# Optimization experiments

Measured on AMD Instinct MI355X. Metric: run time of the kernel, lower is better.

The kernel has to match this reference:

```python
import jax, jax.numpy as jnp
import numpy as np

NEG_CLAMP = -100.0  # torch F.binary_cross_entropy clamps log terms at -100


def _ccl_labels(fg):
    """4-connectivity connected-component labeling of a [H,W] bool mask.
    Labels are assigned in raster-scan first-encounter order, matching
    scipy.ndimage.label with the default structure. Background = 0.
    Implemented as min-index label propagation to a fixed point: each
    component ends up tagged with the min flat index of its pixels (its
    first raster-scan pixel), then roots are ranked by cumsum to get 1..num.
    """
    H, W = fg.shape
    INF = H * W  # sentinel larger than any flat index
    idx = jnp.arange(INF, dtype=jnp.int32).reshape(H, W)
    init = jnp.where(fg, idx, INF)

    def step(x):
        up = jnp.concatenate([x[1:], jnp.full((1, W), INF, x.dtype)], axis=0)
        down = jnp.concatenate([jnp.full((1, W), INF, x.dtype), x[:-1]], axis=0)
        left = jnp.concatenate([x[:, 1:], jnp.full((H, 1), INF, x.dtype)], axis=1)
        right = jnp.concatenate([jnp.full((H, 1), INF, x.dtype), x[:, :-1]], axis=1)
        m = jnp.minimum(jnp.minimum(up, down), jnp.minimum(left, right))
        return jnp.where(fg, jnp.minimum(x, m), INF)

    def cond(carry):
        return carry[1]

    def body(carry):
        x, _ = carry
        nx = step(x)
        return nx, jnp.any(nx != x)

    x, _ = jax.lax.while_loop(cond, body, (init, jnp.array(True)))

    flat = x.reshape(-1)
    fgf = fg.reshape(-1)
    # a pixel is the root of its component iff its propagated tag == its own index
    is_root = fgf & (flat == jnp.arange(INF, dtype=jnp.int32))
    rank = jnp.cumsum(is_root.astype(jnp.int32))  # rank[r] = scipy label of root r
    labels = jnp.where(fgf, rank[jnp.clip(flat, 0, INF - 1)], 0)
    return labels.reshape(H, W)


def _target_map(fg):
    """Replicates: labels == labels.flatten()[1:].argmax() + 1 (faithful to source,
    including its quirky use of argmax position as the selected label value)."""
    labels = _ccl_labels(fg)
    lf = labels.reshape(-1)
    v = jnp.argmax(lf[1:]) + 1  # first occurrence of max, like numpy argmax
    return (labels == v).astype(jnp.float32)


def setup_inputs() -> dict:
    key = jax.random.key(0)
    pred = jax.random.uniform(key, (32, 1, 512, 512), dtype=jnp.float32)
    return {"pred": pred}


def reference(pred):
    fg = pred[:, 0] >= 0.5  # [N,H,W] bool
    target = jax.vmap(_target_map)(fg)[:, None]  # [N,1,H,W] float
    logp = jnp.maximum(jnp.log(pred), NEG_CLAMP)
    log1mp = jnp.maximum(jnp.log1p(-pred), NEG_CLAMP)
    return -jnp.mean(target * logp + (1.0 - target) * log1mp)
```

## Files before the change

kernel.cpp:

```cpp
#include <hip/hip_runtime.h>
#include <math.h>

#define IMG_W 512
#define IMG_H 512
#define HW (IMG_W * IMG_H)
#define LOGHW 18
#define NIMG 32
#define NTOT (NIMG * HW)
#define TILE 64
#define TPI 64
#define NTILE (NIMG * TPI)
#define CPI 64
#define NSCHUNK (NIMG * CPI)
#define VBORD ((8 - 1) * IMG_H)
#define BORD_PER_IMG (VBORD + (8 - 1) * IMG_W)
#define NBORD (NIMG * BORD_PER_IMG)


__device__ __forceinline__ void uf_unite(int* L, int a, int b) {
    while (true) {
        int p = ((volatile int*)L)[a];
        while (p != a) { a = p; p = ((volatile int*)L)[a]; }
        p = ((volatile int*)L)[b];
        while (p != b) { b = p; p = ((volatile int*)L)[b]; }
        if (a == b) return;
        if (a < b) { int t = a; a = b; b = t; }
        int old = atomicMin(&L[a], b);
        if (old == a) return;
        a = old;
    }
}

__global__ __launch_bounds__(512) void k_local(const float* __restrict__ pred,
                                               int* __restrict__ L,
                                               float* __restrict__ partials) {
    __shared__ int lab[TILE * TILE];
    __shared__ float sred[512];
    int tile = blockIdx.x;
    int img = tile >> 6;
    int t = tile & (TPI - 1);
    int ty = t >> 3, tx = t & 7;
    int baseLocal = (ty * TILE) * IMG_W + tx * TILE;
    const float* pi = pred + ((size_t)img << LOGHW);
    int* Li = L + ((size_t)img << LOGHW);
    int tid = threadIdx.x;
    int lane = tid & 63, wave = tid >> 6;

    float acc = 0.0f;
#pragma unroll
    for (int j = 0; j < 8; j++) {
        int row = wave + j * 8;
        float p = pi[baseLocal + row * IMG_W + lane];
        acc += fmaxf(__logf(1.0f - p), -100.0f);
        bool fg = (p >= 0.5f);
        unsigned long long bal = __ballot(fg);
        unsigned long long starts = bal & ~(bal << 1);
        unsigned long long maskle =
            (lane == 63) ? ~0ULL : ((1ULL << (lane + 1)) - 1ULL);
        int lb = -1;
        if (fg) {
            unsigned long long pre = starts & maskle;
            lb = row * TILE + (63 - __builtin_clzll(pre));
        }
        lab[row * TILE + lane] = lb;
    }
    __syncthreads();
#pragma unroll
    for (int j = 0; j < 8; j++) {
        int row = wave + j * 8;
        if (row == 0) continue;
        int i = row * TILE + lane;
        bool c = (lab[i] >= 0) && (lab[i - TILE] >= 0);
        unsigned long long cb = __ballot(c);
        unsigned long long cs = cb & ~(cb << 1);
        if ((cs >> lane) & 1ULL) uf_unite(lab, i, i - TILE);
    }
    __syncthreads();
#pragma unroll
    for (int j = 0; j < 2; j++) {
        int i4 = (tid + j * 512) * 4;
        int ly = i4 >> 6, lx = i4 & 63;
        int4 o;
        int* op = (int*)&o;
#pragma unroll
        for (int k = 0; k < 4; k++) {
            int x = i4 + k;
            int p = lab[x];
            if (p < 0) op[k] = -1;
            else {
                while (p != x) {
                    int g = lab[p];
                    lab[x] = g;
                    x = g;
                    p = lab[x];
                }
                op[k] = baseLocal + (x >> 6) * IMG_W + (x & 63);
            }
        }
        *(int4*)(Li + baseLocal + ly * IMG_W + lx) = o;
    }
    sred[tid] = acc;
    __syncthreads();
    for (int s = 256; s > 0; s >>= 1) {
        if (tid < s) sred[tid] += sred[tid + s];
        __syncthreads();
    }
    if (tid == 0) partials[blockIdx.x] = sred[0];
}

__global__ void k_border(int* __restrict__ L) {
    int gid = blockIdx.x * blockDim.x + threadIdx.x;
    int img = gid / BORD_PER_IMG;
    int r = gid - img * BORD_PER_IMG;
    int* Li = L + ((size_t)img << LOGHW);
    int a, b;
    if (r < VBORD) {
        int k = r >> 9, y = r & 511;
        int x = k * TILE + (TILE - 1);
        a = y * IMG_W + x; b = a + 1;
    } else {
        int r2 = r - VBORD;
        int k = r2 >> 9, x = r2 & 511;
        int y = k * TILE + (TILE - 1);
        a = y * IMG_W + x; b = a + IMG_W;
    }
    bool c = (Li[a] >= 0) && (Li[b] >= 0);
    unsigned long long cb = __ballot(c);
    unsigned long long cs = cb & ~(cb << 1);
    if ((cs >> (threadIdx.x & 63)) & 1ULL) uf_unite(Li, a, b);
}

__global__ __launch_bounds__(256) void k_stats(const int* __restrict__ L,
                                               int* __restrict__ cntArr,
                                               int* __restrict__ maxArr,
                                               int* __restrict__ minArr) {
    __shared__ int s1[256], s2[256], s3[256];
    int chunk = blockIdx.x;
    int img = chunk >> 6;
    int baseL = (chunk & 63) * 4096;
    const int* Li = L + ((size_t)img << LOGHW);
    int t = threadIdx.x;
    int cnt = 0, mx = -1, mn = HW;
#pragma unroll
    for (int j = 0; j < 4; j++) {
        int off = baseL + (t + j * 256) * 4;
        int4 l4 = *(const int4*)(Li + off);
        const int* lp = (const int*)&l4;
#pragma unroll
        for (int k = 0; k < 4; k++) {
            int local = off + k;
            int p = lp[k];
            bool root = (p == local);
            cnt += root ? 1 : 0;
            if (root && local > mx) mx = local;
            if (p >= 0 && local >= 1 && local < mn) mn = local;
        }
    }
    s1[t] = cnt; s2[t] = mx; s3[t] = mn;
    __syncthreads();
    for (int s = 128; s > 0; s >>= 1) {
        if (t < s) {
            s1[t] += s1[t + s];
            s2[t] = max(s2[t], s2[t + s]);
            s3[t] = min(s3[t], s3[t + s]);
        }
        __syncthreads();
    }
    if (t == 0) { cntArr[chunk] = s1[0]; maxArr[chunk] = s2[0]; minArr[chunk] = s3[0]; }
}

__global__ __launch_bounds__(256) void k_rv(const int* __restrict__ cntArr,
                                            const int* __restrict__ maxArr,
                                            const int* __restrict__ minArr,
                                            const int* __restrict__ L,
                                            int* __restrict__ rv) {
    __shared__ int sc[256], sm[256], sn[256];
    __shared__ int sel_chunk, sel_base, result;
    int img = blockIdx.x, t = threadIdx.x;
    int cnt = (t < CPI) ? cntArr[img * CPI + t] : 0;
    sc[t] = cnt;
    sm[t] = (t < CPI) ? maxArr[img * CPI + t] : -1;
    sn[t] = (t < CPI) ? minArr[img * CPI + t] : HW;
    if (t == 0) result = -2;
    __syncthreads();
    for (int off = 1; off < 256; off <<= 1) {
        int v2 = (t >= off) ? sc[t - off] : 0;
        __syncthreads();
        sc[t] += v2;
        __syncthreads();
    }
    int num = sc[255];
    int inc = sc[t], exc = inc - cnt;
    for (int s = 128; s > 0; s >>= 1) {
        if (t < s) { sm[t] = max(sm[t], sm[t + s]); sn[t] = min(sn[t], sn[t + s]); }
        __syncthreads();
    }
    int last_root = sm[0], minFg = sn[0];
    int v;
    if (last_root >= 1) v = last_root;
    else if (last_root == 0) v = (minFg < HW) ? minFg : 1;
    else v = 1;
    if (v >= 1 && v <= num) {
        if (exc < v && v <= inc) { sel_chunk = t; sel_base = exc; }
        __syncthreads();
        int c = sel_chunk, base = sel_base;
        const int* Li = L + ((size_t)img << LOGHW);
        int baseL = c * 4096;
        int f[16];
        int sum = 0;
#pragma unroll
        for (int j = 0; j < 4; j++) {
            int off = baseL + t * 16 + j * 4;
            int4 l4 = *(const int4*)(Li + off);
            const int* lp = (const int*)&l4;
#pragma unroll
            for (int k = 0; k < 4; k++) {
                f[j * 4 + k] = (lp[k] == off + k) ? 1 : 0;
                sum += f[j * 4 + k];
            }
        }
        __syncthreads();
        sc[t] = sum;
        __syncthreads();
        for (int off = 1; off < 256; off <<= 1) {
            int v2 = (t >= off) ? sc[t - off] : 0;
            __syncthreads();
            sc[t] += v2;
            __syncthreads();
        }
        int exc2 = sc[t] - sum;
        int need = v - base;
        if (exc2 < need && need <= sc[t]) {
            int run = exc2;
#pragma unroll
            for (int k = 0; k < 16; k++) {
                run += f[k];
                if (run == need) { result = baseL + t * 16 + k; break; }
            }
        }
        __syncthreads();
    } else {
        __syncthreads();
    }
    if (t == 0) rv[img] = result;
}

__global__ __launch_bounds__(256) void k_loss(const float* __restrict__ pred,
                                              const int* __restrict__ L,
                                              const int* __restrict__ rvArr,
                                              float* __restrict__ partials2) {
    __shared__ float sred[256];
    int blk = blockIdx.x;
    int img = blk >> 6;
    int t = threadIdx.x;
    int rvv = rvArr[img];
    if (rvv < 0) {
        if (t == 0) partials2[blk] = 0.0f;
        return;
    }
    const int* Li = L + ((size_t)img << LOGHW);
    int baseG = blk * 4096;
    float acc = 0.0f;
#pragma unroll
    for (int j = 0; j < 4; j++) {
        int off = baseG + (t + j * 256) * 4;
        float4 p4 = *(const float4*)(pred + off);
        int4 l4 = *(const int4*)(L + off);
        const float* pp = (const float*)&p4;
        const int* lp = (const int*)&l4;
#pragma unroll
        for (int k = 0; k < 4; k++) {
            int p = lp[k];
            if (p < 0) continue;
            int x = p, q = Li[x];
            while (q != x) { x = q; q = Li[x]; }
            if (x == rvv) {
                float pr = pp[k];
                acc += fmaxf(__logf(pr), -100.0f)
                     - fmaxf(__logf(1.0f - pr), -100.0f);
            }
        }
    }
    sred[t] = acc;
    __syncthreads();
    for (int s = 128; s > 0; s >>= 1) {
        if (t < s) sred[t] += sred[t + s];
        __syncthreads();
    }
    if (t == 0) partials2[blk] = sred[0];
}

__global__ __launch_bounds__(256) void k_final(const float* __restrict__ partials,
                                               const float* __restrict__ partials2,
                                               float* __restrict__ out) {
    __shared__ double s[256];
    int t = threadIdx.x;
    double acc = 0.0;
#pragma unroll
    for (int j = 0; j < 8; j++) {
        int idx = t + j * 256;
        acc += (double)partials[idx] + (double)partials2[idx];
    }
    s[t] = acc;
    __syncthreads();
    for (int st = 128; st > 0; st >>= 1) {
        if (t < st) s[t] += s[t + st];
        __syncthreads();
    }
    if (t == 0) out[0] = (float)(-s[0] / (double)NTOT);
}

extern "C" void kernel_launch(void* const* d_in, const int* in_sizes, int n_in,
                              void* d_out, int out_size, void* d_ws, size_t ws_size,
                              hipStream_t stream) {
    const float* pred = (const float*)d_in[0];
    float* out = (float*)d_out;

    char* ws = (char*)d_ws;
    int* L = (int*)ws;
    int* cntArr = (int*)(ws + (size_t)NTOT * 4);
    int* maxArr = cntArr + NSCHUNK;
    int* minArr = maxArr + NSCHUNK;
    float* partials = (float*)(minArr + NSCHUNK);
    float* partials2 = partials + NTILE;
    int* rv = (int*)(partials2 + NSCHUNK);

    k_local<<<dim3(NTILE), dim3(512), 0, stream>>>(pred, L, partials);
    k_border<<<dim3(NBORD / 256), dim3(256), 0, stream>>>(L);
    k_stats<<<dim3(NSCHUNK), dim3(256), 0, stream>>>(L, cntArr, maxArr, minArr);
    k_rv<<<dim3(NIMG), dim3(256), 0, stream>>>(cntArr, maxArr, minArr, L, rv);
    k_loss<<<dim3(NSCHUNK), dim3(256), 0, stream>>>(pred, L, rv, partials2);
    k_final<<<1, dim3(256), 0, stream>>>(partials, partials2, out);
}
```

Baseline: 123.6 us.

## Compact tile-edge roots for border merge and fuse rv, loss and final into one tail

k_local now compresses each run's path to its root in shared memory. It also writes each tile's four edge rows and columns of global root labels into a compact edges buffer. k_border reads these compact per-edge arrays instead of gathering scattered pixels from L. The rv selection, selected-component loss and final reduction are merged into a single 32-block k_tail kernel, which finishes with an atomic counter handled by the last block. This removes two launches and the 2048-block loss pass, but each image's loss scan now runs in a single block over 256K pixels, which may limit parallelism.

```diff
diff --git a/kernel.cpp b/kernel.cpp
--- a/kernel.cpp
+++ b/kernel.cpp
@@ -12,10 +12,8 @@
 #define NTILE (NIMG * TPI)
 #define CPI 64
 #define NSCHUNK (NIMG * CPI)
-#define VBORD ((8 - 1) * IMG_H)
-#define BORD_PER_IMG (VBORD + (8 - 1) * IMG_W)
-#define NBORD (NIMG * BORD_PER_IMG)
-
+#define EDGE_N (NTILE * 64)
+#define NPAIR (NIMG * 112)
 
 __device__ __forceinline__ void uf_unite(int* L, int a, int b) {
     while (true) {
@@ -33,7 +31,9 @@
 
 __global__ __launch_bounds__(512) void k_local(const float* __restrict__ pred,
                                                int* __restrict__ L,
-                                               float* __restrict__ partials) {
+                                               float* __restrict__ partials,
+                                               int* __restrict__ edges,
+                                               unsigned int* __restrict__ counter) {
     __shared__ int lab[TILE * TILE];
     __shared__ float sred[512];
     int tile = blockIdx.x;
@@ -77,6 +77,25 @@
     }
     __syncthreads();
 #pragma unroll
+    for (int j = 0; j < 8; j++) {
+        int row = wave + j * 8;
+        int i = row * TILE + lane;
+        bool fg = (lab[i] >= 0);
+        unsigned long long bal = __ballot(fg);
+        unsigned long long st = bal & ~(bal << 1);
+        if ((st >> lane) & 1ULL) {
+            int x = i, p = lab[x];
+            while (p != x) {
+                int g = lab[p];
+                lab[x] = g;
+                x = g;
+                p = lab[x];
+            }
+            lab[i] = x;
+        }
+    }
+    __syncthreads();
+#pragma unroll
     for (int j = 0; j < 2; j++) {
         int i4 = (tid + j * 512) * 4;
         int ly = i4 >> 6, lx = i4 & 63;
@@ -84,20 +103,29 @@
         int* op = (int*)&o;
 #pragma unroll
         for (int k = 0; k < 4; k++) {
-            int x = i4 + k;
-            int p = lab[x];
-            if (p < 0) op[k] = -1;
+            int s = lab[i4 + k];
+            if (s < 0) op[k] = -1;
             else {
-                while (p != x) {
-                    int g = lab[p];
-                    lab[x] = g;
-                    x = g;
-                    p = lab[x];
-                }
-                op[k] = baseLocal + (x >> 6) * IMG_W + (x & 63);
+                int r = lab[s];
+                op[k] = baseLocal + (r >> 6) * IMG_W + (r & 63);
             }
         }
         *(int4*)(Li + baseLocal + ly * IMG_W + lx) = o;
+    }
+    if (tid < 256) {
+        int e = tid >> 6;
+        int q = tid & 63;
+        int px = (e == 0) ? q
+               : (e == 1) ? (63 * TILE + q)
+               : (e == 2) ? (q * TILE)
+               :            (q * TILE + 63);
+        int s = lab[px];
+        int val = -1;
+        if (s >= 0) {
+            int r = lab[s];
+            val = baseLocal + (r >> 6) * IMG_W + (r & 63);
+        }
+        edges[e * EDGE_N + tile * 64 + q] = val;
     }
     sred[tid] = acc;
     __syncthreads();
@@ -106,28 +134,36 @@
         __syncthreads();
     }
     if (tid == 0) partials[blockIdx.x] = sred[0];
-}
-
-__global__ void k_border(int* __restrict__ L) {
+    if (blockIdx.x == 0 && tid == 0) *counter = 0u;
+}
+
+__global__ __launch_bounds__(256) void k_border(const int* __restrict__ edges,
+                                                int* __restrict__ L) {
     int gid = blockIdx.x * blockDim.x + threadIdx.x;
-    int img = gid / BORD_PER_IMG;
-    int r = gid - img * BORD_PER_IMG;
-    int* Li = L + ((size_t)img << LOGHW);
-    int a, b;
-    if (r < VBORD) {
-        int k = r >> 9, y = r & 511;
-        int x = k * TILE + (TILE - 1);
-        a = y * IMG_W + x; b = a + 1;
+    int pair = gid >> 6;
+    int lane = gid & 63;
+    int a, b, img;
+    if (pair < NIMG * 56) {
+        img = pair / 56;
+        int w = pair - img * 56;
+        int ty = w / 7, tx = w - ty * 7;
+        int tl = img * TPI + ty * 8 + tx;
+        a = edges[3 * EDGE_N + tl * 64 + lane];
+        b = edges[2 * EDGE_N + (tl + 1) * 64 + lane];
     } else {
-        int r2 = r - VBORD;
-        int k = r2 >> 9, x = r2 & 511;
-        int y = k * TILE + (TILE - 1);
-        a = y * IMG_W + x; b = a + IMG_W;
-    }
-    bool c = (Li[a] >= 0) && (Li[b] >= 0);
+        int p2 = pair - NIMG * 56;
+        img = p2 / 56;
+        int w = p2 - img * 56;
+        int ty = w >> 3, tx = w & 7;
+        int tu = img * TPI + ty * 8 + tx;
+        a = edges[1 * EDGE_N + tu * 64 + lane];
+        b = edges[0 * EDGE_N + (tu + 8) * 64 + lane];
+    }
+    bool c = (a >= 0) && (b >= 0);
     unsigned long long cb = __ballot(c);
     unsigned long long cs = cb & ~(cb << 1);
-    if ((cs >> (threadIdx.x & 63)) & 1ULL) uf_unite(Li, a, b);
+    if ((cs >> lane) & 1ULL)
+        uf_unite(L + ((size_t)img << LOGHW), a, b);
 }
 
 __global__ __launch_bounds__(256) void k_stats(const int* __restrict__ L,
@@ -169,14 +205,22 @@
     if (t == 0) { cntArr[chunk] = s1[0]; maxArr[chunk] = s2[0]; minArr[chunk] = s3[0]; }
 }
 
-__global__ __launch_bounds__(256) void k_rv(const int* __restrict__ cntArr,
-                                            const int* __restrict__ maxArr,
-                                            const int* __restrict__ minArr,
-                                            const int* __restrict__ L,
-                                            int* __restrict__ rv) {
+__global__ __launch_bounds__(256) void k_tail(const int* __restrict__ cntArr,
+                                              const int* __restrict__ maxArr,
+                                              const int* __restrict__ minArr,
+                                              const int* __restrict__ L,
+                                              const float* __restrict__ pred,
+                                              const float* __restrict__ partials,
+                                              float* __restrict__ corr,
+                                              unsigned int* __restrict__ counter,
+                                              float* __restrict__ out) {
     __shared__ int sc[256], sm[256], sn[256];
     __shared__ int sel_chunk, sel_base, result;
+    __shared__ float sf[256];
+    __shared__ double sd[256];
+    __shared__ unsigned int oldc;
     int img = blockIdx.x, t = threadIdx.x;
+    const int* Li = L + ((size_t)img << LOGHW);
     int cnt = (t < CPI) ? cntArr[img * CPI + t] : 0;
     sc[t] = cnt;
     sm[t] = (t < CPI) ? maxArr[img * CPI + t] : -1;
@@ -204,7 +248,6 @@
         if (exc < v && v <= inc) { sel_chunk = t; sel_base = exc; }
         __syncthreads();
         int c = sel_chunk, base = sel_base;
-        const int* Li = L + ((size_t)img << LOGHW);
         int baseL = c * 4096;
         int f[16];
         int sum = 0;
@@ -242,72 +285,59 @@
     } else {
         __syncthreads();
     }
-    if (t == 0) rv[img] = result;
-}
-
-__global__ __launch_bounds__(256) void k_loss(const float* __restrict__ pred,
-                                              const int* __restrict__ L,
-                                              const int* __restrict__ rvArr,
-                                              float* __restrict__ partials2) {
-    __shared__ float sred[256];
-    int blk = blockIdx.x;
-    int img = blk >> 6;
-    int t = threadIdx.x;
-    int rvv = rvArr[img];
-    if (rvv < 0) {
-        if (t == 0) partials2[blk] = 0.0f;
-        return;
-    }
-    const int* Li = L + ((size_t)img << LOGHW);
-    int baseG = blk * 4096;
-    float acc = 0.0f;
-#pragma unroll
-    for (int j = 0; j < 4; j++) {
-        int off = baseG + (t + j * 256) * 4;
-        float4 p4 = *(const float4*)(pred + off);
-        int4 l4 = *(const int4*)(L + off);
-        const float* pp = (const float*)&p4;
-        const int* lp = (const int*)&l4;
-#pragma unroll
-        for (int k = 0; k < 4; k++) {
-            int p = lp[k];
-            if (p < 0) continue;
-            int x = p, q = Li[x];
-            while (q != x) { x = q; q = Li[x]; }
-            if (x == rvv) {
-                float pr = pp[k];
-                acc += fmaxf(__logf(pr), -100.0f)
-                     - fmaxf(__logf(1.0f - pr), -100.0f);
-            }
-        }
-    }
-    sred[t] = acc;
+    int rvv = result;
+    float blocksum = 0.0f;
+    if (rvv >= 0) {
+        const float* pi = pred + ((size_t)img << LOGHW);
+        float acc = 0.0f;
+        for (int it = 0; it < HW / 1024; it++) {
+            int off = it * 1024 + t * 4;
+            float4 p4 = *(const float4*)(pi + off);
+            int4 l4 = *(const int4*)(Li + off);
+            const float* pp = (const float*)&p4;
+            const int* lp = (const int*)&l4;
+#pragma unroll
+            for (int k = 0; k < 4; k++) {
+                int p = lp[k];
+                if (p < 0) continue;
+                int x = p, q = Li[x];
+                while (q != x) { x = q; q = Li[x]; }
+                if (x == rvv) {
+                    float pr = pp[k];
+                    acc += fmaxf(__logf(pr), -100.0f)
+                         - fmaxf(__logf(1.0f - pr), -100.0f);
+                }
+            }
+        }
+        sf[t] = acc;
+        __syncthreads();
+        for (int s = 128; s > 0; s >>= 1) {
+            if (t < s) sf[t] += sf[t + s];
+            __syncthreads();
+        }
+        blocksum = sf[0];
+    }
+    if (t == 0) {
+        __hip_atomic_store(&corr[img], blocksum, __ATOMIC_RELAXED,
+                           __HIP_MEMORY_SCOPE_AGENT);
+        oldc = __hip_atomic_fetch_add(counter, 1u, __ATOMIC_ACQ_REL,
+                                      __HIP_MEMORY_SCOPE_AGENT);
+    }
+    __syncthreads();
+    if (oldc != NIMG - 1) return;
+    double acc = 0.0;
+#pragma unroll
+    for (int j = 0; j < 8; j++) acc += (double)partials[t + j * 256];
+    if (t < NIMG)
+        acc += (double)__hip_atomic_load(&corr[t], __ATOMIC_ACQUIRE,
+                                         __HIP_MEMORY_SCOPE_AGENT);
+    sd[t] = acc;
     __syncthreads();
     for (int s = 128; s > 0; s >>= 1) {
-        if (t < s) sred[t] += sred[t + s];
-        __syncthreads();
-    }
-    if (t == 0) partials2[blk] = sred[0];
-}
-
-__global__ __launch_bounds__(256) void k_final(const float* __restrict__ partials,
-                                               const float* __restrict__ partials2,
-                                               float* __restrict__ out) {
-    __shared__ double s[256];
-    int t = threadIdx.x;
-    double acc = 0.0;
-#pragma unroll
-    for (int j = 0; j < 8; j++) {
-        int idx = t + j * 256;
-        acc += (double)partials[idx] + (double)partials2[idx];
-    }
-    s[t] = acc;
-    __syncthreads();
-    for (int st = 128; st > 0; st >>= 1) {
-        if (t < st) s[t] += s[t + st];
-        __syncthreads();
-    }
-    if (t == 0) out[0] = (float)(-s[0] / (double)NTOT);
+        if (t < s) sd[t] += sd[t + s];
+        __syncthreads();
+    }
+    if (t == 0) out[0] = (float)(-sd[0] / (double)NTOT);
 }
 
 extern "C" void kernel_launch(void* const* d_in, const int* in_sizes, int n_in,
@@ -318,17 +348,17 @@
 
     char* ws = (char*)d_ws;
     int* L = (int*)ws;
-    int* cntArr = (int*)(ws + (size_t)NTOT * 4);
+    int* edges = (int*)(ws + (size_t)NTOT * 4);
+    int* cntArr = edges + 4 * EDGE_N;
     int* maxArr = cntArr + NSCHUNK;
     int* minArr = maxArr + NSCHUNK;
     float* partials = (float*)(minArr + NSCHUNK);
-    float* partials2 = partials + NTILE;
-    int* rv = (int*)(partials2 + NSCHUNK);
-
-    k_local<<<dim3(NTILE), dim3(512), 0, stream>>>(pred, L, partials);
-    k_border<<<dim3(NBORD / 256), dim3(256), 0, stream>>>(L);
+    float* corr = partials + NTILE;
+    unsigned int* counter = (unsigned int*)(corr + NIMG);
+
+    k_local<<<dim3(NTILE), dim3(512), 0, stream>>>(pred, L, partials, edges, counter);
+    k_border<<<dim3(NPAIR * 64 / 256), dim3(256), 0, stream>>>(edges, L);
     k_stats<<<dim3(NSCHUNK), dim3(256), 0, stream>>>(L, cntArr, maxArr, minArr);
-    k_rv<<<dim3(NIMG), dim3(256), 0, stream>>>(cntArr, maxArr, minArr, L, rv);
-    k_loss<<<dim3(NSCHUNK), dim3(256), 0, stream>>>(pred, L, rv, partials2);
-    k_final<<<1, dim3(256), 0, stream>>>(partials, partials2, out);
-}
+    k_tail<<<dim3(NIMG), dim3(256), 0, stream>>>(cntArr, maxArr, minArr, L, pred,
+                                                 partials, corr, counter, out);
+}
```

After: 120.1 us, median of 3. 1.03x faster.
